# Kernel optimization log

Measured on AMD Instinct MI355X. Metric: run time of the kernel, lower is better.

The kernel has to match this reference:

```python
import jax, jax.numpy as jnp
import numpy as np

LN_EPS = 1e-5

def setup_inputs() -> dict:
    key = jax.random.key(0)
    ks = jax.random.split(key, 8)
    E, F = 500000, 128
    in_right = jax.random.normal(ks[0], (E, F), dtype=jnp.float32)
    in_left = jax.random.normal(ks[1], (E, F), dtype=jnp.float32)
    # MLP params (torch Linear default init scale ~ 1/sqrt(fan_in))
    W1 = jax.random.normal(ks[2], (2 * F, F), dtype=jnp.float32) / np.sqrt(2 * F)
    b1 = jax.random.normal(ks[3], (F,), dtype=jnp.float32) / np.sqrt(2 * F)
    W2 = jax.random.normal(ks[4], (F, F), dtype=jnp.float32) / np.sqrt(F)
    b2 = jax.random.normal(ks[5], (F,), dtype=jnp.float32) / np.sqrt(F)
    gamma = jnp.ones((F,), dtype=jnp.float32)
    beta = jnp.zeros((F,), dtype=jnp.float32)
    return {"in_right": in_right, "in_left": in_left, "W1": W1, "b1": b1,
            "W2": W2, "b2": b2, "gamma": gamma, "beta": beta}

def reference(in_right, in_left, W1, b1, W2, b2, gamma, beta):
    # msg: [2E, 2F] = stack of (left||right) and (right||left)
    in_lr = jnp.concatenate((in_left, in_right), axis=1)
    in_rl = jnp.concatenate((in_right, in_left), axis=1)
    msg = jnp.concatenate((in_lr, in_rl), axis=0)
    h = jax.nn.relu(msg @ W1 + b1)
    h = jax.nn.relu(h @ W2 + b2)
    # LayerNorm over last dim
    mu = jnp.mean(h, axis=-1, keepdims=True)
    var = jnp.var(h, axis=-1, keepdims=True)
    h = (h - mu) * jax.lax.rsqrt(var + LN_EPS) * gamma + beta
    n_edges = in_right.shape[0]
    return h[:n_edges, :], h[n_edges:, :]
```

## Files before the change

### kernel.cpp

```cpp
#include <hip/hip_runtime.h>
#include <hip/hip_bf16.h>

#define LN_EPS 1e-5f

typedef __attribute__((ext_vector_type(8))) short bf16x8;
typedef __attribute__((ext_vector_type(4))) float f32x4;

__device__ __forceinline__ short f2bf(float x) {
    union { float f; unsigned u; } v; v.f = x;
    unsigned r = v.u + 0x7fff + ((v.u >> 16) & 1);
    return (short)(r >> 16);
}

#define IN_STRIDE 528
#define H_STRIDE  272

__global__ __launch_bounds__(256) void mpnn_mfma(
    const float* __restrict__ inR, const float* __restrict__ inL,
    const float* __restrict__ W1, const float* __restrict__ b1,
    const float* __restrict__ W2, const float* __restrict__ b2,
    const float* __restrict__ gamma, const float* __restrict__ beta,
    float* __restrict__ out, int E, int niters)
{
    __shared__ __align__(16) char inA[32 * IN_STRIDE];
    __shared__ __align__(16) char hbuf[64 * H_STRIDE];
    __shared__ float2 lnp[4][4][16];
    __shared__ __align__(16) float bgl[4][128];

    const int tid  = threadIdx.x;
    const int lane = tid & 63;
    const int wave = tid >> 6;
    const int r    = lane & 15;
    const int q    = lane >> 4;

    if (tid < 128) {
        bgl[0][tid] = b1[tid];
        bgl[1][tid] = b2[tid];
        bgl[2][tid] = gamma[tid];
        bgl[3][tid] = beta[tid];
    }

    bf16x8 A1[2][8], A2[2][4];
#pragma unroll
    for (int t = 0; t < 2; ++t) {
        const int fr = wave * 32 + t * 16 + r;
#pragma unroll
        for (int c = 0; c < 8; ++c)
#pragma unroll
            for (int i = 0; i < 8; ++i)
                A1[t][c][i] = f2bf(W1[(c * 32 + q * 8 + i) * 128 + fr]);
#pragma unroll
        for (int c = 0; c < 4; ++c)
#pragma unroll
            for (int i = 0; i < 8; ++i)
                A2[t][c][i] = f2bf(W2[(c * 32 + q * 8 + i) * 128 + fr]);
    }

    for (int it = blockIdx.x; it < niters; it += gridDim.x) {
        const int e0 = it * 32;
        __syncthreads();

#pragma unroll
        for (int j = 0; j < 4; ++j) {
            const int idx = j * 256 + tid;
            const int e  = idx >> 5;
            const int hw = (idx >> 4) & 1;
            const int c8 = idx & 15;
            int ee = e0 + e; if (ee >= E) ee = E - 1;
            const float* src = hw ? inR : inL;
            const float4 v0 = *(const float4*)(src + (long)ee * 128 + c8 * 8);
            const float4 v1 = *(const float4*)(src + (long)ee * 128 + c8 * 8 + 4);
            bf16x8 s;
            s[0] = f2bf(v0.x); s[1] = f2bf(v0.y); s[2] = f2bf(v0.z); s[3] = f2bf(v0.w);
            s[4] = f2bf(v1.x); s[5] = f2bf(v1.y); s[6] = f2bf(v1.z); s[7] = f2bf(v1.w);
            *(bf16x8*)(&inA[e * IN_STRIDE + hw * 256 + c8 * 16]) = s;
        }
        __syncthreads();

        f32x4 acc[2][4];
#pragma unroll
        for (int t = 0; t < 2; ++t)
#pragma unroll
            for (int u = 0; u < 4; ++u)
                acc[t][u] = f32x4{0.f, 0.f, 0.f, 0.f};
#pragma unroll
        for (int c = 0; c < 8; ++c) {
            const bf16x8 x0 = *(const bf16x8*)(&inA[r        * IN_STRIDE + c * 64 + q * 16]);
            const bf16x8 x1 = *(const bf16x8*)(&inA[(16 + r) * IN_STRIDE + c * 64 + q * 16]);
            const int crl = (c + 4) & 7;
#pragma unroll
            for (int t = 0; t < 2; ++t) {
                acc[t][0] = __builtin_amdgcn_mfma_f32_16x16x32_bf16(A1[t][c],   x0, acc[t][0], 0, 0, 0);
                acc[t][1] = __builtin_amdgcn_mfma_f32_16x16x32_bf16(A1[t][c],   x1, acc[t][1], 0, 0, 0);
                acc[t][2] = __builtin_amdgcn_mfma_f32_16x16x32_bf16(A1[t][crl], x0, acc[t][2], 0, 0, 0);
                acc[t][3] = __builtin_amdgcn_mfma_f32_16x16x32_bf16(A1[t][crl], x1, acc[t][3], 0, 0, 0);
            }
        }

#pragma unroll
        for (int t = 0; t < 2; ++t) {
            const int fq = wave * 32 + t * 16 + q * 4;
            const float4 b1v = *(const float4*)(&bgl[0][fq]);
#pragma unroll
            for (int v = 0; v < 4; ++v) {
                const f32x4 a = acc[t][v];
                short4 s;
                s.x = f2bf(fmaxf(a[0] + b1v.x, 0.f));
                s.y = f2bf(fmaxf(a[1] + b1v.y, 0.f));
                s.z = f2bf(fmaxf(a[2] + b1v.z, 0.f));
                s.w = f2bf(fmaxf(a[3] + b1v.w, 0.f));
                *(short4*)(&hbuf[(v * 16 + r) * H_STRIDE + fq * 2]) = s;
            }
        }
        __syncthreads();

#pragma unroll
        for (int t = 0; t < 2; ++t)
#pragma unroll
            for (int v = 0; v < 4; ++v) acc[t][v] = f32x4{0.f, 0.f, 0.f, 0.f};
#pragma unroll
        for (int c = 0; c < 4; ++c) {
#pragma unroll
            for (int v = 0; v < 4; ++v) {
                const bf16x8 y = *(const bf16x8*)(&hbuf[(v * 16 + r) * H_STRIDE + c * 64 + q * 16]);
#pragma unroll
                for (int t = 0; t < 2; ++t)
                    acc[t][v] = __builtin_amdgcn_mfma_f32_16x16x32_bf16(A2[t][c], y, acc[t][v], 0, 0, 0);
            }
        }

        float s1[4] = {0.f, 0.f, 0.f, 0.f}, s2[4] = {0.f, 0.f, 0.f, 0.f};
#pragma unroll
        for (int t = 0; t < 2; ++t) {
            const int fq = wave * 32 + t * 16 + q * 4;
            const float4 b2v = *(const float4*)(&bgl[1][fq]);
#pragma unroll
            for (int v = 0; v < 4; ++v) {
                f32x4 a = acc[t][v];
                a[0] = fmaxf(a[0] + b2v.x, 0.f);
                a[1] = fmaxf(a[1] + b2v.y, 0.f);
                a[2] = fmaxf(a[2] + b2v.z, 0.f);
                a[3] = fmaxf(a[3] + b2v.w, 0.f);
                acc[t][v] = a;
                s1[v] += a[0] + a[1] + a[2] + a[3];
                s2[v] += a[0] * a[0] + a[1] * a[1] + a[2] * a[2] + a[3] * a[3];
            }
        }
#pragma unroll
        for (int v = 0; v < 4; ++v) {
            s1[v] += __shfl_xor(s1[v], 16);
            s1[v] += __shfl_xor(s1[v], 32);
            s2[v] += __shfl_xor(s2[v], 16);
            s2[v] += __shfl_xor(s2[v], 32);
        }
        if (lane < 16) {
#pragma unroll
            for (int v = 0; v < 4; ++v)
                lnp[wave][v][lane] = make_float2(s1[v], s2[v]);
        }
        __syncthreads();

#pragma unroll
        for (int v = 0; v < 4; ++v) {
            float S1 = 0.f, S2 = 0.f;
#pragma unroll
            for (int w = 0; w < 4; ++w) {
                const float2 p = lnp[w][v][r];
                S1 += p.x; S2 += p.y;
            }
            const float mu  = S1 * (1.f / 128.f);
            const float var = S2 * (1.f / 128.f) - mu * mu;
            const float rs  = rsqrtf(var + LN_EPS);
            const int el = (v & 1) * 16 + r;
            const bool ok = (e0 + el) < E;
            const long orow = ((v < 2) ? 0L : (long)E) + e0 + el;
#pragma unroll
            for (int t = 0; t < 2; ++t) {
                const int fq = wave * 32 + t * 16 + q * 4;
                const float4 gv = *(const float4*)(&bgl[2][fq]);
                const float4 bv = *(const float4*)(&bgl[3][fq]);
                const f32x4 a = acc[t][v];
                float4 o;
                o.x = (a[0] - mu) * rs * gv.x + bv.x;
                o.y = (a[1] - mu) * rs * gv.y + bv.y;
                o.z = (a[2] - mu) * rs * gv.z + bv.z;
                o.w = (a[3] - mu) * rs * gv.w + bv.w;
                if (ok)
                    *(float4*)(out + orow * 128 + fq) = o;
            }
        }
    }
}

extern "C" void kernel_launch(void* const* d_in, const int* in_sizes, int n_in,
                              void* d_out, int out_size, void* d_ws, size_t ws_size,
                              hipStream_t stream) {
    const float* inR   = (const float*)d_in[0];
    const float* inL   = (const float*)d_in[1];
    const float* W1    = (const float*)d_in[2];
    const float* b1    = (const float*)d_in[3];
    const float* W2    = (const float*)d_in[4];
    const float* b2    = (const float*)d_in[5];
    const float* gamma = (const float*)d_in[6];
    const float* beta  = (const float*)d_in[7];
    const int E = in_sizes[0] / 128;

    const int niters = (E + 31) / 32;
    const int d = (niters + 2047) / 2048;
    const int grid = (niters + d - 1) / d;
    mpnn_mfma<<<grid, 256, 0, stream>>>(inR, inL, W1, b1, W2, b2, gamma, beta,
                                        (float*)d_out, E, niters);
}
```

Before: 235.3 us.

## Load inputs straight into MFMA operand registers, drop LDS staging and barriers

Removes the shared-memory staging of the left/right input rows. Each wave now loads its fp32 input fragments from global memory directly into registers, with a two-slot software prefetch across the K chunks, and converts them to bf16 in place. The layer-norm partial-sum buffer is double-buffered by iteration parity, which removes the barrier at the top of the loop as well as the staging barrier. In exchange, all four waves load the same 32 edge rows, so global/L1/L2 load traffic rises about fourfold, and each lane's 32-byte row-strided accesses may coalesce less well than the old cooperative load.

```diff
diff --git a/kernel.cpp b/kernel.cpp
--- a/kernel.cpp
+++ b/kernel.cpp
@@ -11,9 +11,11 @@
     unsigned r = v.u + 0x7fff + ((v.u >> 16) & 1);
     return (short)(r >> 16);
 }
-
-#define IN_STRIDE 528
-#define H_STRIDE  272
+__device__ __forceinline__ short2 cvt2(float a, float b) {
+    short2 p; p.x = f2bf(a); p.y = f2bf(b); return p;
+}
+
+#define H_STRIDE 272
 
 __global__ __launch_bounds__(256) void mpnn_mfma(
     const float* __restrict__ inR, const float* __restrict__ inL,
@@ -22,9 +24,8 @@
     const float* __restrict__ gamma, const float* __restrict__ beta,
     float* __restrict__ out, int E, int niters)
 {
-    __shared__ __align__(16) char inA[32 * IN_STRIDE];
     __shared__ __align__(16) char hbuf[64 * H_STRIDE];
-    __shared__ float2 lnp[4][4][16];
+    __shared__ float2 lnp[2][4][4][16];
     __shared__ __align__(16) float bgl[4][128];
 
     const int tid  = threadIdx.x;
@@ -55,27 +56,14 @@
             for (int i = 0; i < 8; ++i)
                 A2[t][c][i] = f2bf(W2[(c * 32 + q * 8 + i) * 128 + fr]);
     }
-
-    for (int it = blockIdx.x; it < niters; it += gridDim.x) {
+    __syncthreads();
+
+    int par = 0;
+    for (int it = blockIdx.x; it < niters; it += gridDim.x, par ^= 1) {
         const int e0 = it * 32;
-        __syncthreads();
-
-#pragma unroll
-        for (int j = 0; j < 4; ++j) {
-            const int idx = j * 256 + tid;
-            const int e  = idx >> 5;
-            const int hw = (idx >> 4) & 1;
-            const int c8 = idx & 15;
-            int ee = e0 + e; if (ee >= E) ee = E - 1;
-            const float* src = hw ? inR : inL;
-            const float4 v0 = *(const float4*)(src + (long)ee * 128 + c8 * 8);
-            const float4 v1 = *(const float4*)(src + (long)ee * 128 + c8 * 8 + 4);
-            bf16x8 s;
-            s[0] = f2bf(v0.x); s[1] = f2bf(v0.y); s[2] = f2bf(v0.z); s[3] = f2bf(v0.w);
-            s[4] = f2bf(v1.x); s[5] = f2bf(v1.y); s[6] = f2bf(v1.z); s[7] = f2bf(v1.w);
-            *(bf16x8*)(&inA[e * IN_STRIDE + hw * 256 + c8 * 16]) = s;
-        }
-        __syncthreads();
+        long r0 = (long)e0 + r;      if (r0 >= E) r0 = E - 1;
+        long r1 = (long)e0 + 16 + r; if (r1 >= E) r1 = E - 1;
+        const long o0 = r0 * 128, o1 = r1 * 128;
 
         f32x4 acc[2][4];
 #pragma unroll
@@ -83,10 +71,40 @@
 #pragma unroll
             for (int u = 0; u < 4; ++u)
                 acc[t][u] = f32x4{0.f, 0.f, 0.f, 0.f};
+
+        float4 fb[2][4];
+        {
+            const float* s = inL;
+            fb[0][0] = *(const float4*)(s + o0 + q * 8);
+            fb[0][1] = *(const float4*)(s + o0 + q * 8 + 4);
+            fb[0][2] = *(const float4*)(s + o1 + q * 8);
+            fb[0][3] = *(const float4*)(s + o1 + q * 8 + 4);
+        }
 #pragma unroll
         for (int c = 0; c < 8; ++c) {
-            const bf16x8 x0 = *(const bf16x8*)(&inA[r        * IN_STRIDE + c * 64 + q * 16]);
-            const bf16x8 x1 = *(const bf16x8*)(&inA[(16 + r) * IN_STRIDE + c * 64 + q * 16]);
+            if (c < 7) {
+                const int cn = c + 1;
+                const float* s = (cn < 4) ? inL : inR;
+                const int off = (cn & 3) * 32 + q * 8;
+                fb[(c + 1) & 1][0] = *(const float4*)(s + o0 + off);
+                fb[(c + 1) & 1][1] = *(const float4*)(s + o0 + off + 4);
+                fb[(c + 1) & 1][2] = *(const float4*)(s + o1 + off);
+                fb[(c + 1) & 1][3] = *(const float4*)(s + o1 + off + 4);
+            }
+            const float4 a0 = fb[c & 1][0], a1 = fb[c & 1][1];
+            const float4 a2v = fb[c & 1][2], a3v = fb[c & 1][3];
+            bf16x8 x0, x1;
+            {
+                short2 p;
+                p = cvt2(a0.x, a0.y); x0[0] = p.x; x0[1] = p.y;
+                p = cvt2(a0.z, a0.w); x0[2] = p.x; x0[3] = p.y;
+                p = cvt2(a1.x, a1.y); x0[4] = p.x; x0[5] = p.y;
+                p = cvt2(a1.z, a1.w); x0[6] = p.x; x0[7] = p.y;
+                p = cvt2(a2v.x, a2v.y); x1[0] = p.x; x1[1] = p.y;
+                p = cvt2(a2v.z, a2v.w); x1[2] = p.x; x1[3] = p.y;
+                p = cvt2(a3v.x, a3v.y); x1[4] = p.x; x1[5] = p.y;
+                p = cvt2(a3v.z, a3v.w); x1[6] = p.x; x1[7] = p.y;
+            }
             const int crl = (c + 4) & 7;
 #pragma unroll
             for (int t = 0; t < 2; ++t) {
@@ -105,10 +123,9 @@
             for (int v = 0; v < 4; ++v) {
                 const f32x4 a = acc[t][v];
                 short4 s;
-                s.x = f2bf(fmaxf(a[0] + b1v.x, 0.f));
-                s.y = f2bf(fmaxf(a[1] + b1v.y, 0.f));
-                s.z = f2bf(fmaxf(a[2] + b1v.z, 0.f));
-                s.w = f2bf(fmaxf(a[3] + b1v.w, 0.f));
+                short2 p;
+                p = cvt2(fmaxf(a[0] + b1v.x, 0.f), fmaxf(a[1] + b1v.y, 0.f)); s.x = p.x; s.y = p.y;
+                p = cvt2(fmaxf(a[2] + b1v.z, 0.f), fmaxf(a[3] + b1v.w, 0.f)); s.z = p.x; s.w = p.y;
                 *(short4*)(&hbuf[(v * 16 + r) * H_STRIDE + fq * 2]) = s;
             }
         }
@@ -156,7 +173,7 @@
         if (lane < 16) {
 #pragma unroll
             for (int v = 0; v < 4; ++v)
-                lnp[wave][v][lane] = make_float2(s1[v], s2[v]);
+                lnp[par][wave][v][lane] = make_float2(s1[v], s2[v]);
         }
         __syncthreads();
 
@@ -165,7 +182,7 @@
             float S1 = 0.f, S2 = 0.f;
 #pragma unroll
             for (int w = 0; w < 4; ++w) {
-                const float2 p = lnp[w][v][r];
+                const float2 p = lnp[par][w][v][r];
                 S1 += p.x; S2 += p.y;
             }
             const float mu  = S1 * (1.f / 128.f);
```

Result: slower. 428.0 us (+81.9%).

## Split feature dimension across 8 waves per block instead of 4

Applied to the files above, without the earlier changes.

Doubles the block to 512 threads so each wave owns 16 output features instead of 32, halving per-thread resident weight fragments and accumulators. Bias, gamma and beta move from shared memory into registers loaded once per thread. The aim is lower register pressure and more waves per CU to hide global load latency. In exchange, each block reduces LayerNorm partials across 8 waves and has more threads meeting at each barrier per tile.

```diff
diff --git a/kernel.cpp b/kernel.cpp
--- a/kernel.cpp
+++ b/kernel.cpp
@@ -15,7 +15,7 @@
 #define IN_STRIDE 528
 #define H_STRIDE  272
 
-__global__ __launch_bounds__(256) void mpnn_mfma(
+__global__ __launch_bounds__(512) void mpnn_mfma(
     const float* __restrict__ inR, const float* __restrict__ inL,
     const float* __restrict__ W1, const float* __restrict__ b1,
     const float* __restrict__ W2, const float* __restrict__ b2,
@@ -24,8 +24,7 @@
 {
     __shared__ __align__(16) char inA[32 * IN_STRIDE];
     __shared__ __align__(16) char hbuf[64 * H_STRIDE];
-    __shared__ float2 lnp[4][4][16];
-    __shared__ __align__(16) float bgl[4][128];
+    __shared__ float2 lnp[8][4][16];
 
     const int tid  = threadIdx.x;
     const int lane = tid & 63;
@@ -33,27 +32,25 @@
     const int r    = lane & 15;
     const int q    = lane >> 4;
 
-    if (tid < 128) {
-        bgl[0][tid] = b1[tid];
-        bgl[1][tid] = b2[tid];
-        bgl[2][tid] = gamma[tid];
-        bgl[3][tid] = beta[tid];
-    }
-
-    bf16x8 A1[2][8], A2[2][4];
-#pragma unroll
-    for (int t = 0; t < 2; ++t) {
-        const int fr = wave * 32 + t * 16 + r;
+    bf16x8 A1[8], A2[4];
+    float4 b1v, b2v, gv, bv;
+    {
+        const int fr = wave * 16 + r;
 #pragma unroll
         for (int c = 0; c < 8; ++c)
 #pragma unroll
             for (int i = 0; i < 8; ++i)
-                A1[t][c][i] = f2bf(W1[(c * 32 + q * 8 + i) * 128 + fr]);
+                A1[c][i] = f2bf(W1[(c * 32 + q * 8 + i) * 128 + fr]);
 #pragma unroll
         for (int c = 0; c < 4; ++c)
 #pragma unroll
             for (int i = 0; i < 8; ++i)
-                A2[t][c][i] = f2bf(W2[(c * 32 + q * 8 + i) * 128 + fr]);
+                A2[c][i] = f2bf(W2[(c * 32 + q * 8 + i) * 128 + fr]);
+        const int fq = wave * 16 + q * 4;
+        b1v = *(const float4*)(b1 + fq);
+        b2v = *(const float4*)(b2 + fq);
+        gv  = *(const float4*)(gamma + fq);
+        bv  = *(const float4*)(beta + fq);
     }
 
     for (int it = blockIdx.x; it < niters; it += gridDim.x) {
@@ -61,8 +58,8 @@
         __syncthreads();
 
 #pragma unroll
-        for (int j = 0; j < 4; ++j) {
-            const int idx = j * 256 + tid;
+        for (int j = 0; j < 2; ++j) {
+            const int idx = j * 512 + tid;
             const int e  = idx >> 5;
             const int hw = (idx >> 4) & 1;
             const int c8 = idx & 15;
@@ -77,33 +74,26 @@
         }
         __syncthreads();
 
-        f32x4 acc[2][4];
+        f32x4 acc[4];
 #pragma unroll
-        for (int t = 0; t < 2; ++t)
-#pragma unroll
-            for (int u = 0; u < 4; ++u)
-                acc[t][u] = f32x4{0.f, 0.f, 0.f, 0.f};
+        for (int v = 0; v < 4; ++v)
+            acc[v] = f32x4{0.f, 0.f, 0.f, 0.f};
 #pragma unroll
         for (int c = 0; c < 8; ++c) {
             const bf16x8 x0 = *(const bf16x8*)(&inA[r        * IN_STRIDE + c * 64 + q * 16]);
             const bf16x8 x1 = *(const bf16x8*)(&inA[(16 + r) * IN_STRIDE + c * 64 + q * 16]);
             const int crl = (c + 4) & 7;
-#pragma unroll
-            for (int t = 0; t < 2; ++t) {
-                acc[t][0] = __builtin_amdgcn_mfma_f32_16x16x32_bf16(A1[t][c],   x0, acc[t][0], 0, 0, 0);
-                acc[t][1] = __builtin_amdgcn_mfma_f32_16x16x32_bf16(A1[t][c],   x1, acc[t][1], 0, 0, 0);
-                acc[t][2] = __builtin_amdgcn_mfma_f32_16x16x32_bf16(A1[t][crl], x0, acc[t][2], 0, 0, 0);
-                acc[t][3] = __builtin_amdgcn_mfma_f32_16x16x32_bf16(A1[t][crl], x1, acc[t][3], 0, 0, 0);
-            }
+            acc[0] = __builtin_amdgcn_mfma_f32_16x16x32_bf16(A1[c],   x0, acc[0], 0, 0, 0);
+            acc[1] = __builtin_amdgcn_mfma_f32_16x16x32_bf16(A1[c],   x1, acc[1], 0, 0, 0);
+            acc[2] = __builtin_amdgcn_mfma_f32_16x16x32_bf16(A1[crl], x0, acc[2], 0, 0, 0);
+            acc[3] = __builtin_amdgcn_mfma_f32_16x16x32_bf16(A1[crl], x1, acc[3], 0, 0, 0);
         }
 
-#pragma unroll
-        for (int t = 0; t < 2; ++t) {
-            const int fq = wave * 32 + t * 16 + q * 4;
-            const float4 b1v = *(const float4*)(&bgl[0][fq]);
+        {
+            const int fq = wave * 16 + q * 4;
 #pragma unroll
             for (int v = 0; v < 4; ++v) {
-                const f32x4 a = acc[t][v];
+                const f32x4 a = acc[v];
                 short4 s;
                 s.x = f2bf(fmaxf(a[0] + b1v.x, 0.f));
                 s.y = f2bf(fmaxf(a[1] + b1v.y, 0.f));
@@ -115,36 +105,27 @@
         __syncthreads();
 
 #pragma unroll
-        for (int t = 0; t < 2; ++t)
-#pragma unroll
-            for (int v = 0; v < 4; ++v) acc[t][v] = f32x4{0.f, 0.f, 0.f, 0.f};
+        for (int v = 0; v < 4; ++v) acc[v] = f32x4{0.f, 0.f, 0.f, 0.f};
 #pragma unroll
         for (int c = 0; c < 4; ++c) {
 #pragma unroll
             for (int v = 0; v < 4; ++v) {
                 const bf16x8 y = *(const bf16x8*)(&hbuf[(v * 16 + r) * H_STRIDE + c * 64 + q * 16]);
-#pragma unroll
-                for (int t = 0; t < 2; ++t)
-                    acc[t][v] = __builtin_amdgcn_mfma_f32_16x16x32_bf16(A2[t][c], y, acc[t][v], 0, 0, 0);
+                acc[v] = __builtin_amdgcn_mfma_f32_16x16x32_bf16(A2[c], y, acc[v], 0, 0, 0);
             }
         }
 
-        float s1[4] = {0.f, 0.f, 0.f, 0.f}, s2[4] = {0.f, 0.f, 0.f, 0.f};
+        float s1[4], s2[4];
 #pragma unroll
-        for (int t = 0; t < 2; ++t) {
-            const int fq = wave * 32 + t * 16 + q * 4;
-            const float4 b2v = *(const float4*)(&bgl[1][fq]);
-#pragma unroll
-            for (int v = 0; v < 4; ++v) {
-                f32x4 a = acc[t][v];
-                a[0] = fmaxf(a[0] + b2v.x, 0.f);
-                a[1] = fmaxf(a[1] + b2v.y, 0.f);
-                a[2] = fmaxf(a[2] + b2v.z, 0.f);
-                a[3] = fmaxf(a[3] + b2v.w, 0.f);
-                acc[t][v] = a;
-                s1[v] += a[0] + a[1] + a[2] + a[3];
-                s2[v] += a[0] * a[0] + a[1] * a[1] + a[2] * a[2] + a[3] * a[3];
-            }
+        for (int v = 0; v < 4; ++v) {
+            f32x4 a = acc[v];
+            a[0] = fmaxf(a[0] + b2v.x, 0.f);
+            a[1] = fmaxf(a[1] + b2v.y, 0.f);
+            a[2] = fmaxf(a[2] + b2v.z, 0.f);
+            a[3] = fmaxf(a[3] + b2v.w, 0.f);
+            acc[v] = a;
+            s1[v] = a[0] + a[1] + a[2] + a[3];
+            s2[v] = a[0] * a[0] + a[1] * a[1] + a[2] * a[2] + a[3] * a[3];
         }
 #pragma unroll
         for (int v = 0; v < 4; ++v) {
@@ -164,7 +145,7 @@
         for (int v = 0; v < 4; ++v) {
             float S1 = 0.f, S2 = 0.f;
 #pragma unroll
-            for (int w = 0; w < 4; ++w) {
+            for (int w = 0; w < 8; ++w) {
                 const float2 p = lnp[w][v][r];
                 S1 += p.x; S2 += p.y;
             }
@@ -174,20 +155,15 @@
             const int el = (v & 1) * 16 + r;
             const bool ok = (e0 + el) < E;
             const long orow = ((v < 2) ? 0L : (long)E) + e0 + el;
-#pragma unroll
-            for (int t = 0; t < 2; ++t) {
-                const int fq = wave * 32 + t * 16 + q * 4;
-                const float4 gv = *(const float4*)(&bgl[2][fq]);
-                const float4 bv = *(const float4*)(&bgl[3][fq]);
-                const f32x4 a = acc[t][v];
-                float4 o;
-                o.x = (a[0] - mu) * rs * gv.x + bv.x;
-                o.y = (a[1] - mu) * rs * gv.y + bv.y;
-                o.z = (a[2] - mu) * rs * gv.z + bv.z;
-                o.w = (a[3] - mu) * rs * gv.w + bv.w;
-                if (ok)
-                    *(float4*)(out + orow * 128 + fq) = o;
-            }
+            const int fq = wave * 16 + q * 4;
+            const f32x4 a = acc[v];
+            float4 o;
+            o.x = (a[0] - mu) * rs * gv.x + bv.x;
+            o.y = (a[1] - mu) * rs * gv.y + bv.y;
+            o.z = (a[2] - mu) * rs * gv.z + bv.z;
+            o.w = (a[3] - mu) * rs * gv.w + bv.w;
+            if (ok)
+                *(float4*)(out + orow * 128 + fq) = o;
         }
     }
 }
@@ -208,6 +184,6 @@
     const int niters = (E + 31) / 32;
     const int d = (niters + 2047) / 2048;
     const int grid = (niters + d - 1) / d;
-    mpnn_mfma<<<grid, 256, 0, stream>>>(inR, inL, W1, b1, W2, b2, gamma, beta,
+    mpnn_mfma<<<grid, 512, 0, stream>>>(inR, inL, W1, b1, W2, b2, gamma, beta,
                                         (float*)d_out, E, niters);
 }
```

Measured after the change: 243.8 us. 3.6% more time.
